# Kernel optimization log

Hardware: AMD Instinct MI355X
Metric: run time of the kernel (lower is better)

The kernel has to match this reference:

```python
import jax, jax.numpy as jnp
import numpy as np

N, IN_DIM = 50000, 1024
E = 100000
NUM_REL = 40
HEADS, OUT_DIM = 4, 200
HID = HEADS * OUT_DIM  # 800
B = 8192
NEG_SLOPE = 0.2


def setup_inputs() -> dict:
    key = jax.random.key(0)
    ks = jax.random.split(key, 12)
    node_emb = jax.random.normal(ks[0], (N, IN_DIM), dtype=jnp.float32)
    # RelGAT learnable params
    W = jax.random.normal(ks[1], (IN_DIM, HID), dtype=jnp.float32) * (1.0 / np.sqrt(IN_DIM))
    bias = jnp.zeros((HID,), dtype=jnp.float32)
    a_src = jax.random.normal(ks[2], (HEADS, OUT_DIM), dtype=jnp.float32) * 0.1
    a_dst = jax.random.normal(ks[3], (HEADS, OUT_DIM), dtype=jnp.float32) * 0.1
    a_rel = jax.random.normal(ks[4], (HEADS, OUT_DIM), dtype=jnp.float32) * 0.1
    rel_feat = jax.random.normal(ks[5], (NUM_REL, HID), dtype=jnp.float32) * 0.1
    # DistMult scorer relation embeddings
    rel_emb = jax.random.normal(ks[6], (NUM_REL, HID), dtype=jnp.float32) * 0.1
    # Graph structure (constants)
    edge_index = jax.random.randint(ks[7], (2, E), 0, N, dtype=jnp.int64)
    edge_type = jax.random.randint(ks[8], (E,), 0, NUM_REL, dtype=jnp.int64)
    # Triple batch
    src_ids = jax.random.randint(ks[9], (B,), 0, N, dtype=jnp.int64)
    rel_ids = jax.random.randint(ks[10], (B,), 0, NUM_REL, dtype=jnp.int64)
    dst_ids = jax.random.randint(ks[11], (B,), 0, N, dtype=jnp.int64)
    return dict(node_emb=node_emb, W=W, bias=bias, a_src=a_src, a_dst=a_dst,
                a_rel=a_rel, rel_feat=rel_feat, rel_emb=rel_emb,
                edge_index=edge_index, edge_type=edge_type,
                src_ids=src_ids, rel_ids=rel_ids, dst_ids=dst_ids)


def _rel_gat(node_emb, W, bias, a_src, a_dst, a_rel, rel_feat, edge_index, edge_type):
    src, dst = edge_index[0], edge_index[1]
    h = (node_emb @ W).reshape(N, HEADS, OUT_DIM)          # [N,H,D]
    hs = h[src]                                            # [E,H,D] gather
    hd = h[dst]                                            # [E,H,D] gather
    r = rel_feat[edge_type].reshape(E, HEADS, OUT_DIM)     # [E,H,D]
    # relation-conditioned attention logits per head
    logits = (jnp.einsum('ehd,hd->eh', hs, a_src)
              + jnp.einsum('ehd,hd->eh', hd, a_dst)
              + jnp.einsum('ehd,hd->eh', r, a_rel))        # [E,H]
    logits = jax.nn.leaky_relu(logits, NEG_SLOPE)
    # segment softmax over incoming edges of each destination node
    seg_max = jax.ops.segment_max(logits, dst, num_segments=N)   # [N,H]
    e = jnp.exp(logits - seg_max[dst])                           # [E,H]
    denom = jax.ops.segment_sum(e, dst, num_segments=N)          # [N,H]
    alpha = e / denom[dst]                                       # [E,H]
    # weighted scatter-aggregate of source messages
    out = jax.ops.segment_sum(alpha[:, :, None] * hs, dst, num_segments=N)  # [N,H,D]
    return out.reshape(N, HID) + bias                            # dropout: eval mode (identity)


def reference(node_emb, W, bias, a_src, a_dst, a_rel, rel_feat, rel_emb,
              edge_index, edge_type, src_ids, rel_ids, dst_ids):
    refined = _rel_gat(node_emb, W, bias, a_src, a_dst, a_rel, rel_feat,
                       edge_index, edge_type)                # [N, HID]
    src_vec = refined[src_ids]                               # [B, HID]
    dst_vec = refined[dst_ids]                               # [B, HID]
    # DistMult: sum(s * r * d)
    scores = jnp.sum(src_vec * rel_emb[rel_ids] * dst_vec, axis=-1)  # [B]
    return scores
```

## Files before the change

### kernel.cpp

```cpp
#include <hip/hip_runtime.h>
#include <hip/hip_bf16.h>
#include <math.h>

#define NN 50000
#define IN_DIM 1024
#define EE 100000
#define NUM_REL 40
#define HEADS 4
#define OUT_D 200
#define HID 800
#define BB 8192
#define SLOT_CAP 16384
#define SRC_CAP 50176
#define WT_COLS 896

typedef __attribute__((ext_vector_type(8))) short short8;
typedef __attribute__((ext_vector_type(4))) float f32x4;

__device__ inline unsigned short f2bf(float f) {
    unsigned int u = __float_as_uint(f);
    u += 0x7FFF + ((u >> 16) & 1);
    return (unsigned short)(u >> 16);
}
__device__ inline float bf2f(unsigned short s) {
    return __uint_as_float(((unsigned int)s) << 16);
}
__device__ inline void gl2lds16(const unsigned short* g, unsigned short* l) {
    __builtin_amdgcn_global_load_lds(
        (const __attribute__((address_space(1))) void*)g,
        (__attribute__((address_space(3))) void*)l, 16, 0, 0);
}

__device__ inline int wave_compact(bool won, int* ctr) {
    unsigned long long m = __ballot(won);
    if (!m) return -1;
    int lane = threadIdx.x & 63;
    int leader = __ffsll((long long)m) - 1;
    int base = 0;
    if (lane == leader) base = atomicAdd(ctr, __popcll(m));
    base = __shfl(base, leader, 64);
    return won ? base + __popcll(m & ((1ull << lane) - 1)) : -1;
}

#define INIT_BLOCKS 196
__global__ __launch_bounds__(256) void k_init_wa(int* slot_of_node, int* xrow_of_node,
                                                 int* deg, int* counters,
                                                 const float* W, const float* a_src,
                                                 const float* a_dst, const float* a_rel,
                                                 const float* rel_feat, float* Wa, float* prel) {
    int b = blockIdx.x;
    if (b < INIT_BLOCKS) {
        int i = b * 256 + threadIdx.x;
        if (i < NN) { slot_of_node[i] = -1; xrow_of_node[i] = -1; }
        if (i < SLOT_CAP) deg[i] = 0;
        if (i < 8) counters[i] = 0;
        return;
    }
    int wid = (b - INIT_BLOCKS) * 4 + (threadIdx.x >> 6);
    int lane = threadIdx.x & 63;
    if (wid >= IN_DIM * 8 + NUM_REL * HEADS) return;
    float acc = 0.f;
    int d = lane * 4;
    if (d < OUT_D) {
        const float* row;
        const float* a;
        if (wid < IN_DIM * 8) {
            int k = wid >> 3, c = wid & 7;
            int h = c & 3;
            row = W + (size_t)k * HID + h * OUT_D;
            a = ((c < 4) ? a_src : a_dst) + h * OUT_D;
        } else {
            int j = wid - IN_DIM * 8;
            int r = j >> 2, h = j & 3;
            row = rel_feat + (size_t)r * HID + h * OUT_D;
            a = a_rel + h * OUT_D;
        }
        float4 wv = *(const float4*)(row + d);
        float4 av = *(const float4*)(a + d);
        acc = wv.x * av.x + wv.y * av.y + wv.z * av.z + wv.w * av.w;
    }
    for (int off = 32; off; off >>= 1) acc += __shfl_down(acc, off, 64);
    if (lane == 0) {
        if (wid < IN_DIM * 8) Wa[wid] = acc;
        else prel[wid - IN_DIM * 8] = acc;
    }
}

__global__ void k_build_slots(const int* src_ids, const int* dst_ids,
                              int* slot_of_node, int* counters, int* scorelist) {
    int i = blockIdx.x * 256 + threadIdx.x;
    bool valid = i < 2 * BB;
    int n = 0;
    bool won = false;
    if (valid) {
        n = (i < BB) ? src_ids[i] : dst_ids[i - BB];
        if (slot_of_node[n] == -1)
            won = (atomicCAS(&slot_of_node[n], -1, -2) == -1);
    }
    int s = wave_compact(won, &counters[0]);
    if (won) {
        slot_of_node[n] = s;
        scorelist[s] = n;
    }
}

__global__ void k_edge0(const int* ei, const int* slot_of_node,
                        int* xrow_of_node, int* counters, int* rows, int* deg) {
    int e = blockIdx.x * 256 + threadIdx.x;
    bool valid = e < EE;
    int slot = -1, sn = 0;
    if (valid) {
        int dn = ei[EE + e];
        slot = slot_of_node[dn];
    }
    bool surv = valid && slot >= 0;
    bool won = false;
    if (surv) {
        sn = ei[e];
        if (xrow_of_node[sn] == -1)
            won = (atomicCAS(&xrow_of_node[sn], -1, -2) == -1);
    }
    int t = wave_compact(won, &counters[1]);
    if (won) {
        rows[t] = sn;
        xrow_of_node[sn] = t;
    }
    if (surv) atomicAdd(&deg[slot], 1);
}

__global__ __launch_bounds__(256) void k_tail_scan(const int* scorelist, int* xrow_of_node,
                                                   int* counters, int* rows,
                                                   const int* deg, int* base, int* cursor) {
    int t = threadIdx.x;
    if (blockIdx.x == 0) {
        __shared__ int pref[257];
        int s = 0;
        const int4* dv = (const int4*)(deg + t * (SLOT_CAP / 256));
        for (int i = 0; i < SLOT_CAP / 256 / 4; ++i) {
            int4 v = dv[i];
            s += v.x + v.y + v.z + v.w;
        }
        pref[t + 1] = s;
        if (t == 0) pref[0] = 0;
        __syncthreads();
        if (t == 0)
            for (int i = 1; i <= 256; ++i) pref[i] += pref[i - 1];
        __syncthreads();
        int r = pref[t];
        for (int i = 0; i < SLOT_CAP / 256; ++i) {
            int idx = t * (SLOT_CAP / 256) + i;
            base[idx] = r;
            cursor[idx] = r;
            r += deg[idx];
        }
        return;
    }
    int i = (blockIdx.x - 1) * 256 + t;
    bool valid = i < counters[0];
    int n = 0;
    bool won = false;
    if (valid) {
        n = scorelist[i];
        won = (xrow_of_node[n] < 0);
    }
    int tt = wave_compact(won, &counters[3]);
    if (won) {
        int xr = counters[1] + tt;
        xrow_of_node[n] = xr;
        rows[xr] = n;
    }
}

#define WT_BLOCKS 224
#define GATHER_BLOCKS 3584
__global__ __launch_bounds__(256) void k_gather_wt(const float* x, const int* rows,
                                                   const int* counters, unsigned short* xg,
                                                   const float* W, const float* Wa,
                                                   unsigned short* Wt) {
    int t = threadIdx.x;
    if (blockIdx.x < WT_BLOCKS) {
        __shared__ float tile[64][65];
        int b = blockIdx.x;
        int k0 = (b & 15) * 64, c0 = (b >> 4) * 64;
        {
            int kk = t >> 2, cc = (t & 3) * 16;
            for (int i = 0; i < 16; ++i) {
                int c = c0 + cc + i;
                float v = 0.f;
                if (c < HID) v = W[(size_t)(k0 + kk) * HID + c];
                else if (c < HID + 8) v = Wa[(size_t)(k0 + kk) * 8 + (c - HID)];
                tile[cc + i][kk] = v;
            }
        }
        __syncthreads();
        {
            int cc = t >> 2, kk = (t & 3) * 16;
            unsigned short o[16];
            for (int i = 0; i < 16; ++i) o[i] = f2bf(tile[cc][kk + i]);
            *(short8*)(Wt + (size_t)(c0 + cc) * IN_DIM + k0 + kk) = *(short8*)o;
            *(short8*)(Wt + (size_t)(c0 + cc) * IN_DIM + k0 + kk + 8) = *(short8*)(o + 8);
        }
        return;
    }
    int nneed = counters[1] + counters[3];
    int lim = nneed * 128;
    for (int gid = (blockIdx.x - WT_BLOCKS) * 256 + t; gid < lim;
         gid += GATHER_BLOCKS * 256) {
        int row = gid >> 7;
        int j = (gid & 127) * 8;
        int node = rows[row];
        const float* src = x + (size_t)node * IN_DIM + j;
        float4 a = *(const float4*)(src);
        float4 b = *(const float4*)(src + 4);
        unsigned short o[8] = {f2bf(a.x), f2bf(a.y), f2bf(a.z), f2bf(a.w),
                               f2bf(b.x), f2bf(b.y), f2bf(b.z), f2bf(b.w)};
        *(short8*)(xg + (size_t)row * IN_DIM + j) = *(short8*)o;
    }
}

#define GBM 128
#define GBN 128
#define GBK 64
__global__ __launch_bounds__(256) void k_hgemm(const unsigned short* xg, const unsigned short* Wt,
                                               const int* counters, unsigned short* h_src,
                                               float* sS, float* sD) {
    int nsrc = counters[1];
    int nneed = nsrc + counters[3];
    int lin = blockIdx.x + 7 * blockIdx.y;
    int g = lin / 56, r = lin % 56;
    int rowb = g * 8 + (r & 7);
    int colb = r >> 3;
    int col0 = colb * GBN;
    int row0 = rowb * GBM;
    int rowlim = (col0 == 768) ? nneed : nsrc;
    if (row0 >= rowlim) return;
    __shared__ unsigned short As[GBM * GBK];
    __shared__ unsigned short Bs[GBN * GBK];
    int t = threadIdx.x;
    int crow = ((t >> 6) << 4) + (t & 15), coff = ((t >> 4) & 3) << 3;
    const unsigned short* a0 = xg + (size_t)(row0 + crow) * IN_DIM + coff;
    const unsigned short* a1 = a0 + (size_t)64 * IN_DIM;
    const unsigned short* b0 = Wt + (size_t)(col0 + crow) * IN_DIM + coff;
    const unsigned short* b1 = b0 + (size_t)64 * IN_DIM;
    unsigned short* la0 = As + t * 8;
    unsigned short* la1 = As + (256 + t) * 8;
    unsigned short* la2 = As + (512 + t) * 8;
    unsigned short* la3 = As + (768 + t) * 8;
    unsigned short* lb0 = Bs + t * 8;
    unsigned short* lb1 = Bs + (256 + t) * 8;
    unsigned short* lb2 = Bs + (512 + t) * 8;
    unsigned short* lb3 = Bs + (768 + t) * 8;
    int w = t >> 6, lane = t & 63;
    int ga = (w >> 1) * 4, gb = (w & 1) * 4;
    int wr = (w >> 1) * 64, wc = (w & 1) * 64;
    int fm = lane & 15, fq = lane >> 4;
    f32x4 acc[4][4] = {};
    for (int k0 = 0; k0 < IN_DIM; k0 += GBK) {
        __syncthreads();
        gl2lds16(a0 + k0, la0);
        gl2lds16(a1 + k0, la1);
        gl2lds16(a0 + k0 + 32, la2);
        gl2lds16(a1 + k0 + 32, la3);
        gl2lds16(b0 + k0, lb0);
        gl2lds16(b1 + k0, lb1);
        gl2lds16(b0 + k0 + 32, lb2);
        gl2lds16(b1 + k0 + 32, lb3);
        __syncthreads();
#pragma unroll
        for (int s = 0; s < 2; ++s) {
            short8 af[4], bf[4];
#pragma unroll
            for (int i = 0; i < 4; ++i)
                af[i] = *(const short8*)&As[(s * 512 + (ga + i) * 64 + lane) * 8];
#pragma unroll
            for (int j = 0; j < 4; ++j)
                bf[j] = *(const short8*)&Bs[(s * 512 + (gb + j) * 64 + lane) * 8];
#pragma unroll
            for (int i = 0; i < 4; ++i)
#pragma unroll
                for (int j = 0; j < 4; ++j)
                    acc[i][j] = __builtin_amdgcn_mfma_f32_16x16x32_bf16(af[i], bf[j], acc[i][j], 0, 0, 0);
        }
    }
#pragma unroll
    for (int i = 0; i < 4; ++i) {
#pragma unroll
        for (int j = 0; j < 4; ++j) {
            int gcol = col0 + wc + j * 16 + fm;
            if (gcol >= HID + 8) continue;
#pragma unroll
            for (int rr = 0; rr < 4; ++rr) {
                int grow = row0 + wr + i * 16 + fq * 4 + rr;
                float v = acc[i][j][rr];
                if (gcol < HID) {
                    if (grow < nsrc) h_src[(size_t)grow * HID + gcol] = f2bf(v);
                } else if (grow < nneed) {
                    int c = gcol - HID;
                    if (c < 4) sS[grow * 4 + c] = v;
                    else sD[grow * 4 + (c - 4)] = v;
                }
            }
        }
    }
}

__global__ void k_place(const int* ei, const int* etype, const int* slot_of_node,
                        const int* xrow_of_node, int* cursor,
                        const float* sS, const float* sD, const float* prel,
                        float* clogit, int* tlist) {
    int e = blockIdx.x * 256 + threadIdx.x;
    if (e >= EE) return;
    int dn = ei[EE + e];
    int slot = slot_of_node[dn];
    if (slot < 0) return;
    int sn = ei[e];
    int r = etype[e];
    int xs = xrow_of_node[sn];
    int xd = xrow_of_node[dn];
    int pos = atomicAdd(&cursor[slot], 1);
    tlist[pos] = xs;
    float4 lg;
    float* lp = (float*)&lg;
#pragma unroll
    for (int h = 0; h < 4; ++h) {
        float v = sS[xs * 4 + h] + sD[xd * 4 + h] + prel[r * 4 + h];
        lp[h] = v > 0.f ? v : 0.2f * v;
    }
    *(float4*)&clogit[(size_t)pos * 4] = lg;
}

__global__ __launch_bounds__(256) void k_aggregate(const int* counters, const int* base,
                                                   const int* deg, const int* tlist,
                                                   const float* clogit,
                                                   const unsigned short* h_src, const float* bias,
                                                   float* refined) {
    int b = blockIdx.x;
    if (b >= counters[0]) return;
    int beg = base[b], d = deg[b];
    __shared__ float m4[4], den4[4];
    __shared__ float alpha[64][4];
    __shared__ int tsl[64];
    int t = threadIdx.x;
    if (t < 4) {
        float m = -3e38f;
        for (int j = 0; j < d; ++j)
            m = fmaxf(m, clogit[(size_t)(beg + j) * 4 + t]);
        float s = 0.f;
        for (int j = 0; j < d; ++j)
            s += expf(clogit[(size_t)(beg + j) * 4 + t] - m);
        m4[t] = m;
        den4[t] = s;
    }
    __syncthreads();
    int h0 = t / 200, h1 = (t + 256) / 200, h2 = (t + 512) / 200;
    float acc0 = 0.f, acc1 = 0.f, acc2 = 0.f, acc3 = 0.f;
    for (int j0 = 0; j0 < d; j0 += 64) {
        int nc = min(64, d - j0);
        if (t < nc * 4) {
            int j = t >> 2, h = t & 3;
            alpha[j][h] = expf(clogit[(size_t)(beg + j0 + j) * 4 + h] - m4[h]) / den4[h];
            if (h == 0) tsl[j] = tlist[beg + j0 + j];
        }
        __syncthreads();
        for (int j = 0; j < nc; ++j) {
            const unsigned short* hr = h_src + (size_t)tsl[j] * HID;
            acc0 += alpha[j][h0] * bf2f(hr[t]);
            acc1 += alpha[j][h1] * bf2f(hr[t + 256]);
            acc2 += alpha[j][h2] * bf2f(hr[t + 512]);
            if (t < 32) acc3 += alpha[j][3] * bf2f(hr[768 + t]);
        }
        __syncthreads();
    }
    float* rr = refined + (size_t)b * HID;
    rr[t] = acc0 + bias[t];
    rr[t + 256] = acc1 + bias[t + 256];
    rr[t + 512] = acc2 + bias[t + 512];
    if (t < 32) rr[768 + t] = acc3 + bias[768 + t];
}

__global__ __launch_bounds__(256) void k_score(const int* src_ids, const int* rel_ids,
                                               const int* dst_ids, const int* slot_of_node,
                                               const float* rel_emb, const float* refined,
                                               float* out) {
    int gid = blockIdx.x * 256 + threadIdx.x;
    int b = gid >> 6;
    int lane = threadIdx.x & 63;
    if (b >= BB) return;
    int ss = slot_of_node[src_ids[b]];
    int ds = slot_of_node[dst_ids[b]];
    int r = rel_ids[b];
    const float* sv = refined + (size_t)ss * HID;
    const float* dv = refined + (size_t)ds * HID;
    const float* rv = rel_emb + (size_t)r * HID;
    float acc = 0.f;
    for (int c4 = lane; c4 < 200; c4 += 64) {
        float4 s = *(const float4*)(sv + c4 * 4);
        float4 dq = *(const float4*)(dv + c4 * 4);
        float4 rr = *(const float4*)(rv + c4 * 4);
        acc += s.x * rr.x * dq.x + s.y * rr.y * dq.y + s.z * rr.z * dq.z + s.w * rr.w * dq.w;
    }
    for (int off = 32; off; off >>= 1) acc += __shfl_down(acc, off, 64);
    if (lane == 0) out[b] = acc;
}

extern "C" void kernel_launch(void* const* d_in, const int* in_sizes, int n_in,
                              void* d_out, int out_size, void* d_ws, size_t ws_size,
                              hipStream_t stream) {
    const float* node_emb = (const float*)d_in[0];
    const float* W        = (const float*)d_in[1];
    const float* bias     = (const float*)d_in[2];
    const float* a_src    = (const float*)d_in[3];
    const float* a_dst    = (const float*)d_in[4];
    const float* a_rel    = (const float*)d_in[5];
    const float* rel_feat = (const float*)d_in[6];
    const float* rel_emb  = (const float*)d_in[7];
    const int* edge_index = (const int*)d_in[8];
    const int* edge_type  = (const int*)d_in[9];
    const int* src_ids    = (const int*)d_in[10];
    const int* rel_ids    = (const int*)d_in[11];
    const int* dst_ids    = (const int*)d_in[12];
    float* out = (float*)d_out;

    char* w = (char*)d_ws;
    auto alloc = [&](size_t bytes) -> void* {
        void* p = (void*)w;
        w += (bytes + 255) & ~(size_t)255;
        return p;
    };
    int* slot_of_node = (int*)alloc((size_t)NN * 4);
    int* xrow_of_node = (int*)alloc((size_t)NN * 4);
    int* scorelist    = (int*)alloc((size_t)SLOT_CAP * 4);
    int* rows         = (int*)alloc((size_t)NN * 4);
    int* counters     = (int*)alloc(256);
    int* deg          = (int*)alloc((size_t)SLOT_CAP * 4);
    int* base         = (int*)alloc((size_t)SLOT_CAP * 4);
    int* cursor       = (int*)alloc((size_t)SLOT_CAP * 4);
    int* tlist        = (int*)alloc((size_t)EE * 4);
    float* clogit = (float*)alloc((size_t)EE * 4 * 4);
    float* sS     = (float*)alloc((size_t)SRC_CAP * 4 * 4);
    float* sD     = (float*)alloc((size_t)SRC_CAP * 4 * 4);
    float* Wa     = (float*)alloc((size_t)IN_DIM * 8 * 4);
    float* prel   = (float*)alloc((size_t)NUM_REL * 4 * 4);
    unsigned short* xg    = (unsigned short*)alloc((size_t)SRC_CAP * IN_DIM * 2);
    unsigned short* Wt    = (unsigned short*)alloc((size_t)WT_COLS * IN_DIM * 2);
    unsigned short* h_src = (unsigned short*)alloc((size_t)SRC_CAP * HID * 2);
    float* refined = (float*)alloc((size_t)SLOT_CAP * HID * 4);

    int wa_blocks = (IN_DIM * 8 + NUM_REL * HEADS + 3) / 4;
    k_init_wa<<<INIT_BLOCKS + wa_blocks, 256, 0, stream>>>(
        slot_of_node, xrow_of_node, deg, counters,
        W, a_src, a_dst, a_rel, rel_feat, Wa, prel);
    k_build_slots<<<(2 * BB + 255) / 256, 256, 0, stream>>>(src_ids, dst_ids, slot_of_node,
                                                            counters, scorelist);
    k_edge0<<<(EE + 255) / 256, 256, 0, stream>>>(edge_index, slot_of_node,
                                                  xrow_of_node, counters, rows, deg);
    k_tail_scan<<<1 + SLOT_CAP / 256, 256, 0, stream>>>(scorelist, xrow_of_node, counters,
                                                        rows, deg, base, cursor);
    k_gather_wt<<<WT_BLOCKS + GATHER_BLOCKS, 256, 0, stream>>>(
        node_emb, rows, counters, xg, W, Wa, Wt);
    dim3 ggrid(WT_COLS / GBN, (SRC_CAP + GBM - 1) / GBM);
    k_hgemm<<<ggrid, 256, 0, stream>>>(xg, Wt, counters, h_src, sS, sD);
    k_place<<<(EE + 255) / 256, 256, 0, stream>>>(edge_index, edge_type, slot_of_node,
                                                  xrow_of_node, cursor, sS, sD, prel,
                                                  clogit, tlist);
    k_aggregate<<<SLOT_CAP, 256, 0, stream>>>(counters, base, deg, tlist,
                                              clogit, h_src, bias, refined);
    k_score<<<(BB * 64 + 255) / 256, 256, 0, stream>>>(src_ids, rel_ids, dst_ids,
                                                       slot_of_node, rel_emb, refined, out);
}
```

Baseline: 506.3 us.

## Double-buffer 256x128 GEMM tile with 512 threads and vectorize aggregation loads

The h GEMM moves to a 256-row tile computed by 512 threads (8 waves). A ping-pong LDS double buffer issues the next K-slice's global-to-LDS loads while MFMAs run on the current one, using vmcnt waits and bare barriers, and s_setprio raises priority around the MFMA block. Separately, the aggregation kernel now has 200 threads each read 4 bf16 values with one ushort4 load and write a float4, replacing scalar per-element loads. The GEMM changes trade more LDS and registers per block for less load latency exposure. In the aggregation kernel 56 of the 256 threads now sit idle.

```diff
diff --git a/kernel.cpp b/kernel.cpp
--- a/kernel.cpp
+++ b/kernel.cpp
@@ -218,10 +218,44 @@
     }
 }
 
-#define GBM 128
+#define GBM 256
 #define GBN 128
 #define GBK 64
-__global__ __launch_bounds__(256) void k_hgemm(const unsigned short* xg, const unsigned short* Wt,
+
+#define STAGE(AS, BS, K0) do {                                          \
+    gl2lds16(aP0 + (K0),      (AS) + (size_t)(0 * 512 + t) * 8);        \
+    gl2lds16(aP1 + (K0),      (AS) + (size_t)(1 * 512 + t) * 8);        \
+    gl2lds16(aP0 + (K0) + 32, (AS) + (size_t)(2 * 512 + t) * 8);        \
+    gl2lds16(aP1 + (K0) + 32, (AS) + (size_t)(3 * 512 + t) * 8);        \
+    gl2lds16(bP  + (K0),      (BS) + (size_t)(0 * 512 + t) * 8);        \
+    gl2lds16(bP  + (K0) + 32, (BS) + (size_t)(1 * 512 + t) * 8);        \
+} while (0)
+
+#define COMPUTE(AS, BS) do {                                            \
+    _Pragma("unroll")                                                   \
+    for (int s = 0; s < 2; ++s) {                                       \
+        short8 af[4], bf4[4];                                           \
+        _Pragma("unroll")                                               \
+        for (int i = 0; i < 4; ++i)                                     \
+            af[i] = *(const short8*)&(AS)[(size_t)(s * 1024 + (gm + i) * 64 + lane) * 8]; \
+        _Pragma("unroll")                                               \
+        for (int j = 0; j < 4; ++j)                                     \
+            bf4[j] = *(const short8*)&(BS)[(size_t)(s * 512 + (gn + j) * 64 + lane) * 8]; \
+        __builtin_amdgcn_s_setprio(1);                                  \
+        _Pragma("unroll")                                               \
+        for (int i = 0; i < 4; ++i)                                     \
+            _Pragma("unroll")                                           \
+            for (int j = 0; j < 4; ++j)                                 \
+                acc[i][j] = __builtin_amdgcn_mfma_f32_16x16x32_bf16(af[i], bf4[j], acc[i][j], 0, 0, 0); \
+        __builtin_amdgcn_s_setprio(0);                                  \
+    }                                                                   \
+} while (0)
+
+#define GATE6 asm volatile("s_waitcnt vmcnt(6)\n\ts_barrier" ::: "memory")
+#define GATE0 asm volatile("s_waitcnt vmcnt(0)\n\ts_barrier" ::: "memory")
+#define BARX  asm volatile("s_barrier" ::: "memory")
+
+__global__ __launch_bounds__(512) void k_hgemm(const unsigned short* xg, const unsigned short* Wt,
                                                const int* counters, unsigned short* h_src,
                                                float* sS, float* sD) {
     int nsrc = counters[1];
@@ -234,53 +268,36 @@
     int row0 = rowb * GBM;
     int rowlim = (col0 == 768) ? nneed : nsrc;
     if (row0 >= rowlim) return;
-    __shared__ unsigned short As[GBM * GBK];
-    __shared__ unsigned short Bs[GBN * GBK];
+    __shared__ unsigned short As0[GBM * GBK];
+    __shared__ unsigned short As1[GBM * GBK];
+    __shared__ unsigned short Bs0[GBN * GBK];
+    __shared__ unsigned short Bs1[GBN * GBK];
     int t = threadIdx.x;
-    int crow = ((t >> 6) << 4) + (t & 15), coff = ((t >> 4) & 3) << 3;
-    const unsigned short* a0 = xg + (size_t)(row0 + crow) * IN_DIM + coff;
-    const unsigned short* a1 = a0 + (size_t)64 * IN_DIM;
-    const unsigned short* b0 = Wt + (size_t)(col0 + crow) * IN_DIM + coff;
-    const unsigned short* b1 = b0 + (size_t)64 * IN_DIM;
-    unsigned short* la0 = As + t * 8;
-    unsigned short* la1 = As + (256 + t) * 8;
-    unsigned short* la2 = As + (512 + t) * 8;
-    unsigned short* la3 = As + (768 + t) * 8;
-    unsigned short* lb0 = Bs + t * 8;
-    unsigned short* lb1 = Bs + (256 + t) * 8;
-    unsigned short* lb2 = Bs + (512 + t) * 8;
-    unsigned short* lb3 = Bs + (768 + t) * 8;
+    int rb = ((t >> 6) << 4) + (t & 15);
+    int kb = ((t >> 4) & 3) << 3;
+    const unsigned short* aP0 = xg + (size_t)(row0 + rb) * IN_DIM + kb;
+    const unsigned short* aP1 = aP0 + (size_t)128 * IN_DIM;
+    const unsigned short* bP  = Wt + (size_t)(col0 + rb) * IN_DIM + kb;
     int w = t >> 6, lane = t & 63;
-    int ga = (w >> 1) * 4, gb = (w & 1) * 4;
+    int gm = (w >> 1) * 4, gn = (w & 1) * 4;
     int wr = (w >> 1) * 64, wc = (w & 1) * 64;
     int fm = lane & 15, fq = lane >> 4;
     f32x4 acc[4][4] = {};
-    for (int k0 = 0; k0 < IN_DIM; k0 += GBK) {
-        __syncthreads();
-        gl2lds16(a0 + k0, la0);
-        gl2lds16(a1 + k0, la1);
-        gl2lds16(a0 + k0 + 32, la2);
-        gl2lds16(a1 + k0 + 32, la3);
-        gl2lds16(b0 + k0, lb0);
-        gl2lds16(b1 + k0, lb1);
-        gl2lds16(b0 + k0 + 32, lb2);
-        gl2lds16(b1 + k0 + 32, lb3);
-        __syncthreads();
-#pragma unroll
-        for (int s = 0; s < 2; ++s) {
-            short8 af[4], bf[4];
-#pragma unroll
-            for (int i = 0; i < 4; ++i)
-                af[i] = *(const short8*)&As[(s * 512 + (ga + i) * 64 + lane) * 8];
-#pragma unroll
-            for (int j = 0; j < 4; ++j)
-                bf[j] = *(const short8*)&Bs[(s * 512 + (gb + j) * 64 + lane) * 8];
-#pragma unroll
-            for (int i = 0; i < 4; ++i)
-#pragma unroll
-                for (int j = 0; j < 4; ++j)
-                    acc[i][j] = __builtin_amdgcn_mfma_f32_16x16x32_bf16(af[i], bf[j], acc[i][j], 0, 0, 0);
-        }
+    STAGE(As0, Bs0, 0);
+#pragma unroll 1
+    for (int kk = 0; kk < 16; kk += 2) {
+        STAGE(As1, Bs1, (kk + 1) * 64);
+        GATE6;
+        COMPUTE(As0, Bs0);
+        BARX;
+        if (kk < 14) {
+            STAGE(As0, Bs0, (kk + 2) * 64);
+            GATE6;
+        } else {
+            GATE0;
+        }
+        COMPUTE(As1, Bs1);
+        BARX;
     }
 #pragma unroll
     for (int i = 0; i < 4; ++i) {
@@ -352,8 +369,8 @@
         den4[t] = s;
     }
     __syncthreads();
-    int h0 = t / 200, h1 = (t + 256) / 200, h2 = (t + 512) / 200;
-    float acc0 = 0.f, acc1 = 0.f, acc2 = 0.f, acc3 = 0.f;
+    int head = t / 50;
+    float4 acc = {0.f, 0.f, 0.f, 0.f};
     for (int j0 = 0; j0 < d; j0 += 64) {
         int nc = min(64, d - j0);
         if (t < nc * 4) {
@@ -362,20 +379,23 @@
             if (h == 0) tsl[j] = tlist[beg + j0 + j];
         }
         __syncthreads();
-        for (int j = 0; j < nc; ++j) {
-            const unsigned short* hr = h_src + (size_t)tsl[j] * HID;
-            acc0 += alpha[j][h0] * bf2f(hr[t]);
-            acc1 += alpha[j][h1] * bf2f(hr[t + 256]);
-            acc2 += alpha[j][h2] * bf2f(hr[t + 512]);
-            if (t < 32) acc3 += alpha[j][3] * bf2f(hr[768 + t]);
+        if (t < 200) {
+            for (int j = 0; j < nc; ++j) {
+                float a = alpha[j][head];
+                ushort4 hv = *(const ushort4*)(h_src + (size_t)tsl[j] * HID + t * 4);
+                acc.x += a * bf2f(hv.x);
+                acc.y += a * bf2f(hv.y);
+                acc.z += a * bf2f(hv.z);
+                acc.w += a * bf2f(hv.w);
+            }
         }
         __syncthreads();
     }
-    float* rr = refined + (size_t)b * HID;
-    rr[t] = acc0 + bias[t];
-    rr[t + 256] = acc1 + bias[t + 256];
-    rr[t + 512] = acc2 + bias[t + 512];
-    if (t < 32) rr[768 + t] = acc3 + bias[768 + t];
+    if (t < 200) {
+        float4 bv = *(const float4*)(bias + t * 4);
+        float4 o = {acc.x + bv.x, acc.y + bv.y, acc.z + bv.z, acc.w + bv.w};
+        *(float4*)(refined + (size_t)b * HID + t * 4) = o;
+    }
 }
 
 __global__ __launch_bounds__(256) void k_score(const int* src_ids, const int* rel_ids,
@@ -458,8 +478,8 @@
                                                         rows, deg, base, cursor);
     k_gather_wt<<<WT_BLOCKS + GATHER_BLOCKS, 256, 0, stream>>>(
         node_emb, rows, counters, xg, W, Wa, Wt);
-    dim3 ggrid(WT_COLS / GBN, (SRC_CAP + GBM - 1) / GBM);
-    k_hgemm<<<ggrid, 256, 0, stream>>>(xg, Wt, counters, h_src, sS, sD);
+    dim3 ggrid(7, 200);
+    k_hgemm<<<ggrid, 512, 0, stream>>>(xg, Wt, counters, h_src, sS, sD);
     k_place<<<(EE + 255) / 256, 256, 0, stream>>>(edge_index, edge_type, slot_of_node,
                                                   xrow_of_node, cursor, sS, sD, prel,
                                                   clogit, tlist);
```

Result: no change. 504.1 us (-0.4%).
